# Kernel tuning notes

Measured on AMD Instinct MI355X. Metric: run time of the kernel, lower is better.

The kernel has to match this reference:

```python
import jax, jax.numpy as jnp
import numpy as np

SH_C0 = 0.28209479177387814
SH_C1 = 0.4886025119029199
SH_C2 = (1.0925484305920792, -1.0925484305920792, 0.31539156525252005,
         -1.0925484305920792, 0.5462742152960396)
EPS = 1e-6


def eval_sh_bases2(d):
    # d: (..., 3) unit directions -> (..., 9) degree-2 real SH basis
    x, y, z = d[..., 0], d[..., 1], d[..., 2]
    return jnp.stack([
        jnp.full(x.shape, SH_C0, d.dtype),
        -SH_C1 * y, SH_C1 * z, -SH_C1 * x,
        SH_C2[0] * x * y, SH_C2[1] * y * z,
        SH_C2[2] * (2.0 * z * z - x * x - y * y),
        SH_C2[3] * x * z, SH_C2[4] * (x * x - y * y)], axis=-1)


def get_sh_weights(x, sh_feats, transforms, locs):
    # x: [N,3]; transforms: [J,4,4]; sh_feats: [J,9]; locs: [J,3] -> weights [N,J]
    N = x.shape[0]
    xh = jnp.concatenate([x, jnp.ones((N, 1), x.dtype)], axis=-1)  # [N,4]
    # per-joint transform of every point (replaces python loop of bmm)
    xj = jnp.einsum('jab,nb->jna', transforms, xh)[..., :3]        # [J,N,3]
    vdirs = locs[:, None, :] - xj                                   # [J,N,3]
    lengths = jnp.linalg.norm(vdirs, axis=-1)                       # [J,N]
    vdirs = vdirs / lengths[..., None]
    sh_mult = eval_sh_bases2(vdirs)                                 # [J,N,9]
    rads = jax.nn.relu(jnp.sum(sh_mult * sh_feats[:, None, :], axis=-1) + 0.5)  # [J,N]
    rel = jax.nn.relu(1.0 - lengths / jnp.maximum(rads, EPS))
    rel = jnp.where(rads < EPS, 0.0, rel)                           # non_valid -> 0
    return rel.T                                                    # [N,J]


def weighted_transformation(pts, weights, transforms):
    # pts: [M,3]; weights: [M,J]; transforms: [J,4,4] -> blended points [M,3]
    M = pts.shape[0]
    ph = jnp.concatenate([pts, jnp.ones((M, 1), pts.dtype)], axis=-1)  # [M,4]
    tp = jnp.einsum('jab,mb->mja', transforms, ph)[..., :3]            # [M,J,3]
    wsum = jnp.sum(weights, axis=-1, keepdims=True)                    # [M,1]
    wn = weights / jnp.maximum(wsum, EPS)
    blended = jnp.einsum('mj,mjd->md', wn, tp)                         # [M,3]
    return jnp.where(wsum > EPS, blended, pts)


def setup_inputs() -> dict:
    key = jax.random.key(0)
    ks = jax.random.split(key, 5)
    B, S, J = 2048, 128, 24
    return {
        'xyz_sampled': jax.random.normal(ks[0], (B, S, 3), jnp.float32),
        'viewdirs': jax.random.normal(ks[1], (B, S, 3), jnp.float32),
        'transforms': jax.random.normal(ks[2], (J, 4, 4), jnp.float32),
        'sh_feats': jax.random.normal(ks[3], (J, 9), jnp.float32),
        'locs': jax.random.normal(ks[4], (J, 3), jnp.float32),
    }


def reference(xyz_sampled, viewdirs, transforms, sh_feats, locs):
    B, S, _ = xyz_sampled.shape
    x = xyz_sampled.reshape(-1, 3)
    N = x.shape[0]
    tmp = jnp.concatenate([x, (xyz_sampled - viewdirs).reshape(-1, 3)], axis=0)  # [2N,3]
    w = get_sh_weights(x, sh_feats, transforms, locs)   # [N,J]
    w2 = jnp.concatenate([w, w], axis=0)                # [2N,J]
    out = weighted_transformation(tmp, w2, transforms)  # [2N,3]
    xyz_out = out[:N].reshape(B, S, 3)
    vd_out = (out[:N] - out[N:]).reshape(B, S, 3)
    return xyz_out, vd_out
```

## Files before the change

kernel.cpp:

```cpp
#include <hip/hip_runtime.h>

#define NJ 24
#define EPSF 1e-6f

__global__ __launch_bounds__(256) void shCaster_kernel(
    const float* __restrict__ xyz,
    const float* __restrict__ vdirs,
    const float* __restrict__ transforms,
    const float* __restrict__ sh_feats,
    const float* __restrict__ locs,
    float* __restrict__ out,
    int N)
{
    constexpr float SH_C0 = 0.28209479177387814f;
    constexpr float SH_C1 = 0.4886025119029199f;
    constexpr float C2_0 = 1.0925484305920792f;
    constexpr float C2_1 = -1.0925484305920792f;
    constexpr float C2_2 = 0.31539156525252005f;
    constexpr float C2_3 = -1.0925484305920792f;
    constexpr float C2_4 = 0.5462742152960396f;

    __shared__ float sT[NJ * 12];
    __shared__ float sF[NJ * 9];
    __shared__ float sL[NJ * 3];

    const int tid = threadIdx.x;
    for (int i = tid; i < NJ * 16; i += 256) {
        int j = i >> 4, rc = i & 15, r = rc >> 2, c = rc & 3;
        if (r < 3) sT[j * 12 + r * 4 + c] = transforms[i];
    }
    if (tid < NJ * 9)  sF[tid] = sh_feats[tid];
    if (tid < NJ * 3)  sL[tid] = locs[tid];
    __syncthreads();

    int n = blockIdx.x * 256 + tid;
    if (n >= N) return;

    const float x0 = xyz[3 * n + 0];
    const float x1 = xyz[3 * n + 1];
    const float x2 = xyz[3 * n + 2];
    const float v0 = vdirs[3 * n + 0];
    const float v1 = vdirs[3 * n + 1];
    const float v2 = vdirs[3 * n + 2];

    float wsum = 0.0f;
    float A[12];
#pragma unroll
    for (int k = 0; k < 12; ++k) A[k] = 0.0f;

#pragma unroll 4
    for (int j = 0; j < NJ; ++j) {
        const float* T = &sT[j * 12];
        float p0 = T[0] * x0 + T[1] * x1 + T[2]  * x2 + T[3];
        float p1 = T[4] * x0 + T[5] * x1 + T[6]  * x2 + T[7];
        float p2 = T[8] * x0 + T[9] * x1 + T[10] * x2 + T[11];
        float d0 = sL[j * 3 + 0] - p0;
        float d1 = sL[j * 3 + 1] - p1;
        float d2 = sL[j * 3 + 2] - p2;
        float len2 = d0 * d0 + d1 * d1 + d2 * d2;
        float rlen = rsqrtf(fmaxf(len2, 1e-30f));
        float len  = len2 * rlen;
        float dx = d0 * rlen, dy = d1 * rlen, dz = d2 * rlen;

        const float* F = &sF[j * 9];
        float dot = SH_C0 * F[0]
                  - SH_C1 * dy * F[1]
                  + SH_C1 * dz * F[2]
                  - SH_C1 * dx * F[3]
                  + C2_0 * (dx * dy) * F[4]
                  + C2_1 * (dy * dz) * F[5]
                  + C2_2 * (2.0f * dz * dz - dx * dx - dy * dy) * F[6]
                  + C2_3 * (dx * dz) * F[7]
                  + C2_4 * (dx * dx - dy * dy) * F[8];
        float rads = fmaxf(dot + 0.5f, 0.0f);
        float rel  = fmaxf(1.0f - __fdividef(len, fmaxf(rads, EPSF)), 0.0f);
        rel = (rads < EPSF) ? 0.0f : rel;

        wsum += rel;
#pragma unroll
        for (int k = 0; k < 12; ++k) A[k] += rel * T[k];
    }

    const float inv = __fdividef(1.0f, fmaxf(wsum, EPSF));
    float bx0 = (A[0] * x0 + A[1] * x1 + A[2]  * x2 + A[3])  * inv;
    float bx1 = (A[4] * x0 + A[5] * x1 + A[6]  * x2 + A[7])  * inv;
    float bx2 = (A[8] * x0 + A[9] * x1 + A[10] * x2 + A[11]) * inv;
    float bv0 = (A[0] * v0 + A[1] * v1 + A[2]  * v2) * inv;
    float bv1 = (A[4] * v0 + A[5] * v1 + A[6]  * v2) * inv;
    float bv2 = (A[8] * v0 + A[9] * v1 + A[10] * v2) * inv;

    const bool valid = wsum > EPSF;
    float o0 = valid ? bx0 : x0;
    float o1 = valid ? bx1 : x1;
    float o2 = valid ? bx2 : x2;
    float w0 = valid ? bv0 : v0;
    float w1 = valid ? bv1 : v1;
    float w2 = valid ? bv2 : v2;

    out[3 * n + 0] = o0;
    out[3 * n + 1] = o1;
    out[3 * n + 2] = o2;
    float* outv = out + 3LL * N;
    outv[3 * n + 0] = w0;
    outv[3 * n + 1] = w1;
    outv[3 * n + 2] = w2;
}

extern "C" void kernel_launch(void* const* d_in, const int* in_sizes, int n_in,
                              void* d_out, int out_size, void* d_ws, size_t ws_size,
                              hipStream_t stream) {
    const float* xyz        = (const float*)d_in[0];
    const float* vdirs      = (const float*)d_in[1];
    const float* transforms = (const float*)d_in[2];
    const float* sh_feats   = (const float*)d_in[3];
    const float* locs       = (const float*)d_in[4];
    float* out = (float*)d_out;

    const int N = in_sizes[0] / 3;
    if (N <= 0) return;
    const int threads = 256;
    const int blocks = (N + threads - 1) / threads;
    shCaster_kernel<<<blocks, threads, 0, stream>>>(
        xyz, vdirs, transforms, sh_feats, locs, out, N);
}
```

Baseline: 82.43 us.

## Process two points per thread and read joint params directly from global memory

Each thread now handles two points, so every joint's transform, SH coefficients and location are loaded once and reused across both points. The shared-memory staging and block barrier are removed; parameters come straight from global memory as uniform, cache-resident loads. The SH constants are folded into per-joint coefficients and the dot product is written as an explicit fma chain. This roughly doubles accumulator registers per thread and halves the number of blocks, which may reduce occupancy and latency hiding.

After: 79.54 us. -3.5%, faster.

```diff
diff --git a/kernel.cpp b/kernel.cpp
--- a/kernel.cpp
+++ b/kernel.cpp
@@ -2,8 +2,10 @@
 
 #define NJ 24
 #define EPSF 1e-6f
+#define PPT 2
+#define TPB 256
 
-__global__ __launch_bounds__(256) void shCaster_kernel(
+__global__ __launch_bounds__(TPB) void shCaster_kernel(
     const float* __restrict__ xyz,
     const float* __restrict__ vdirs,
     const float* __restrict__ transforms,
@@ -14,96 +16,119 @@
 {
     constexpr float SH_C0 = 0.28209479177387814f;
     constexpr float SH_C1 = 0.4886025119029199f;
-    constexpr float C2_0 = 1.0925484305920792f;
-    constexpr float C2_1 = -1.0925484305920792f;
-    constexpr float C2_2 = 0.31539156525252005f;
-    constexpr float C2_3 = -1.0925484305920792f;
-    constexpr float C2_4 = 0.5462742152960396f;
+    constexpr float C2_0  = 1.0925484305920792f;
+    constexpr float C2_2  = 0.31539156525252005f;
+    constexpr float C2_4  = 0.5462742152960396f;
 
-    __shared__ float sT[NJ * 12];
-    __shared__ float sF[NJ * 9];
-    __shared__ float sL[NJ * 3];
+    const int tid  = threadIdx.x;
+    const int base = blockIdx.x * (TPB * PPT) + tid;
 
-    const int tid = threadIdx.x;
-    for (int i = tid; i < NJ * 16; i += 256) {
-        int j = i >> 4, rc = i & 15, r = rc >> 2, c = rc & 3;
-        if (r < 3) sT[j * 12 + r * 4 + c] = transforms[i];
-    }
-    if (tid < NJ * 9)  sF[tid] = sh_feats[tid];
-    if (tid < NJ * 3)  sL[tid] = locs[tid];
-    __syncthreads();
+    int   idx[PPT];
+    bool  act[PPT];
+    float X[PPT][3], V[PPT][3], A[PPT][12], wsum[PPT];
 
-    int n = blockIdx.x * 256 + tid;
-    if (n >= N) return;
-
-    const float x0 = xyz[3 * n + 0];
-    const float x1 = xyz[3 * n + 1];
-    const float x2 = xyz[3 * n + 2];
-    const float v0 = vdirs[3 * n + 0];
-    const float v1 = vdirs[3 * n + 1];
-    const float v2 = vdirs[3 * n + 2];
-
-    float wsum = 0.0f;
-    float A[12];
 #pragma unroll
-    for (int k = 0; k < 12; ++k) A[k] = 0.0f;
-
-#pragma unroll 4
-    for (int j = 0; j < NJ; ++j) {
-        const float* T = &sT[j * 12];
-        float p0 = T[0] * x0 + T[1] * x1 + T[2]  * x2 + T[3];
-        float p1 = T[4] * x0 + T[5] * x1 + T[6]  * x2 + T[7];
-        float p2 = T[8] * x0 + T[9] * x1 + T[10] * x2 + T[11];
-        float d0 = sL[j * 3 + 0] - p0;
-        float d1 = sL[j * 3 + 1] - p1;
-        float d2 = sL[j * 3 + 2] - p2;
-        float len2 = d0 * d0 + d1 * d1 + d2 * d2;
-        float rlen = rsqrtf(fmaxf(len2, 1e-30f));
-        float len  = len2 * rlen;
-        float dx = d0 * rlen, dy = d1 * rlen, dz = d2 * rlen;
-
-        const float* F = &sF[j * 9];
-        float dot = SH_C0 * F[0]
-                  - SH_C1 * dy * F[1]
-                  + SH_C1 * dz * F[2]
-                  - SH_C1 * dx * F[3]
-                  + C2_0 * (dx * dy) * F[4]
-                  + C2_1 * (dy * dz) * F[5]
-                  + C2_2 * (2.0f * dz * dz - dx * dx - dy * dy) * F[6]
-                  + C2_3 * (dx * dz) * F[7]
-                  + C2_4 * (dx * dx - dy * dy) * F[8];
-        float rads = fmaxf(dot + 0.5f, 0.0f);
-        float rel  = fmaxf(1.0f - __fdividef(len, fmaxf(rads, EPSF)), 0.0f);
-        rel = (rads < EPSF) ? 0.0f : rel;
-
-        wsum += rel;
+    for (int p = 0; p < PPT; ++p) {
+        const int n = base + p * TPB;
+        act[p] = (n < N);
+        const int m = act[p] ? n : 0;
+        idx[p] = m;
+        X[p][0] = xyz[3 * m + 0];
+        X[p][1] = xyz[3 * m + 1];
+        X[p][2] = xyz[3 * m + 2];
+        V[p][0] = vdirs[3 * m + 0];
+        V[p][1] = vdirs[3 * m + 1];
+        V[p][2] = vdirs[3 * m + 2];
+        wsum[p] = 0.0f;
 #pragma unroll
-        for (int k = 0; k < 12; ++k) A[k] += rel * T[k];
+        for (int k = 0; k < 12; ++k) A[p][k] = 0.0f;
     }
 
-    const float inv = __fdividef(1.0f, fmaxf(wsum, EPSF));
-    float bx0 = (A[0] * x0 + A[1] * x1 + A[2]  * x2 + A[3])  * inv;
-    float bx1 = (A[4] * x0 + A[5] * x1 + A[6]  * x2 + A[7])  * inv;
-    float bx2 = (A[8] * x0 + A[9] * x1 + A[10] * x2 + A[11]) * inv;
-    float bv0 = (A[0] * v0 + A[1] * v1 + A[2]  * v2) * inv;
-    float bv1 = (A[4] * v0 + A[5] * v1 + A[6]  * v2) * inv;
-    float bv2 = (A[8] * v0 + A[9] * v1 + A[10] * v2) * inv;
+#pragma unroll 8
+    for (int j = 0; j < NJ; ++j) {
+        const float4 T0 = *reinterpret_cast<const float4*>(transforms + j * 16 + 0);
+        const float4 T1 = *reinterpret_cast<const float4*>(transforms + j * 16 + 4);
+        const float4 T2 = *reinterpret_cast<const float4*>(transforms + j * 16 + 8);
 
-    const bool valid = wsum > EPSF;
-    float o0 = valid ? bx0 : x0;
-    float o1 = valid ? bx1 : x1;
-    float o2 = valid ? bx2 : x2;
-    float w0 = valid ? bv0 : v0;
-    float w1 = valid ? bv1 : v1;
-    float w2 = valid ? bv2 : v2;
+        const float* Fj = sh_feats + j * 9;
+        const float G0 =  SH_C0 * Fj[0];
+        const float G1 = -SH_C1 * Fj[1];
+        const float G2 =  SH_C1 * Fj[2];
+        const float G3 = -SH_C1 * Fj[3];
+        const float G4 =  C2_0  * Fj[4];
+        const float G5 = -C2_0  * Fj[5];
+        const float G6 =  C2_2  * Fj[6];
+        const float G7 = -C2_0  * Fj[7];
+        const float G8 =  C2_4  * Fj[8];
 
-    out[3 * n + 0] = o0;
-    out[3 * n + 1] = o1;
-    out[3 * n + 2] = o2;
-    float* outv = out + 3LL * N;
-    outv[3 * n + 0] = w0;
-    outv[3 * n + 1] = w1;
-    outv[3 * n + 2] = w2;
+        const float L0 = locs[j * 3 + 0];
+        const float L1 = locs[j * 3 + 1];
+        const float L2 = locs[j * 3 + 2];
+
+#pragma unroll
+        for (int p = 0; p < PPT; ++p) {
+            const float px = fmaf(T0.x, X[p][0], fmaf(T0.y, X[p][1], fmaf(T0.z, X[p][2], T0.w)));
+            const float py = fmaf(T1.x, X[p][0], fmaf(T1.y, X[p][1], fmaf(T1.z, X[p][2], T1.w)));
+            const float pz = fmaf(T2.x, X[p][0], fmaf(T2.y, X[p][1], fmaf(T2.z, X[p][2], T2.w)));
+
+            const float d0 = L0 - px, d1 = L1 - py, d2 = L2 - pz;
+            const float len2 = fmaf(d0, d0, fmaf(d1, d1, d2 * d2));
+            const float rlen = rsqrtf(fmaxf(len2, 1e-30f));
+            const float len  = len2 * rlen;
+            const float dx = d0 * rlen, dy = d1 * rlen, dz = d2 * rlen;
+
+            const float xx = dx * dx, yy = dy * dy, zz = dz * dz;
+            float dot = fmaf(G1, dy, G0);
+            dot = fmaf(G2, dz, dot);
+            dot = fmaf(G3, dx, dot);
+            dot = fmaf(G4, dx * dy, dot);
+            dot = fmaf(G5, dy * dz, dot);
+            dot = fmaf(G7, dx * dz, dot);
+            dot = fmaf(G6, fmaf(2.0f, zz, -(xx + yy)), dot);
+            dot = fmaf(G8, xx - yy, dot);
+
+            const float rads = fmaxf(dot + 0.5f, 0.0f);
+            float rel = fmaxf(1.0f - __fdividef(len, fmaxf(rads, EPSF)), 0.0f);
+            rel = (rads < EPSF) ? 0.0f : rel;
+
+            wsum[p] += rel;
+            A[p][0]  = fmaf(rel, T0.x, A[p][0]);
+            A[p][1]  = fmaf(rel, T0.y, A[p][1]);
+            A[p][2]  = fmaf(rel, T0.z, A[p][2]);
+            A[p][3]  = fmaf(rel, T0.w, A[p][3]);
+            A[p][4]  = fmaf(rel, T1.x, A[p][4]);
+            A[p][5]  = fmaf(rel, T1.y, A[p][5]);
+            A[p][6]  = fmaf(rel, T1.z, A[p][6]);
+            A[p][7]  = fmaf(rel, T1.w, A[p][7]);
+            A[p][8]  = fmaf(rel, T2.x, A[p][8]);
+            A[p][9]  = fmaf(rel, T2.y, A[p][9]);
+            A[p][10] = fmaf(rel, T2.z, A[p][10]);
+            A[p][11] = fmaf(rel, T2.w, A[p][11]);
+        }
+    }
+
+#pragma unroll
+    for (int p = 0; p < PPT; ++p) {
+        if (!act[p]) continue;
+        const int n = idx[p];
+        const float inv = __fdividef(1.0f, fmaxf(wsum[p], EPSF));
+
+        const float bx0 = fmaf(A[p][0], X[p][0], fmaf(A[p][1], X[p][1], fmaf(A[p][2],  X[p][2], A[p][3])))  * inv;
+        const float bx1 = fmaf(A[p][4], X[p][0], fmaf(A[p][5], X[p][1], fmaf(A[p][6],  X[p][2], A[p][7])))  * inv;
+        const float bx2 = fmaf(A[p][8], X[p][0], fmaf(A[p][9], X[p][1], fmaf(A[p][10], X[p][2], A[p][11]))) * inv;
+        const float bv0 = fmaf(A[p][0], V[p][0], fmaf(A[p][1], V[p][1], A[p][2]  * V[p][2])) * inv;
+        const float bv1 = fmaf(A[p][4], V[p][0], fmaf(A[p][5], V[p][1], A[p][6]  * V[p][2])) * inv;
+        const float bv2 = fmaf(A[p][8], V[p][0], fmaf(A[p][9], V[p][1], A[p][10] * V[p][2])) * inv;
+
+        const bool valid = wsum[p] > EPSF;
+        out[3 * n + 0] = valid ? bx0 : X[p][0];
+        out[3 * n + 1] = valid ? bx1 : X[p][1];
+        out[3 * n + 2] = valid ? bx2 : X[p][2];
+        float* outv = out + 3LL * N;
+        outv[3 * n + 0] = valid ? bv0 : V[p][0];
+        outv[3 * n + 1] = valid ? bv1 : V[p][1];
+        outv[3 * n + 2] = valid ? bv2 : V[p][2];
+    }
 }
 
 extern "C" void kernel_launch(void* const* d_in, const int* in_sizes, int n_in,
@@ -118,8 +143,8 @@
 
     const int N = in_sizes[0] / 3;
     if (N <= 0) return;
-    const int threads = 256;
-    const int blocks = (N + threads - 1) / threads;
-    shCaster_kernel<<<blocks, threads, 0, stream>>>(
+    const int pts_per_block = TPB * PPT;
+    const int blocks = (N + pts_per_block - 1) / pts_per_block;
+    shCaster_kernel<<<blocks, TPB, 0, stream>>>(
         xyz, vdirs, transforms, sh_feats, locs, out, N);
 }
```
